# Optimization experiments

Hardware: AMD Instinct MI355X
Metric: run time of the kernel (lower is better)

Reference implementation:

```python
import jax, jax.numpy as jnp
import numpy as np

B, N, F, E, K, R, H = 16, 2048, 2048, 128, 10, 2, 2


def setup_inputs() -> dict:
    key = jax.random.key(0)
    ks = jax.random.split(key, 11)
    s = 0.1  # keep embeddings close so the Gaussian kernel does not underflow
    rel = jax.random.normal(ks[0], (B, E), jnp.float32) * s
    arg1 = jax.random.normal(ks[1], (B, E), jnp.float32) * s
    arg2 = jax.random.normal(ks[2], (B, E), jnp.float32) * s
    fact_rel = jax.random.normal(ks[3], (B, F, E), jnp.float32) * s
    fact_arg1 = jax.random.normal(ks[4], (B, F, E), jnp.float32) * s
    fact_arg2 = jax.random.normal(ks[5], (B, F, E), jnp.float32) * s
    entity_embeddings = jax.random.normal(ks[6], (B, N, E), jnp.float32) * s
    hop_W = jax.random.normal(ks[7], (R, H, E, E), jnp.float32) / jnp.sqrt(jnp.float32(E))
    hop_b = jax.random.normal(ks[8], (R, H, E), jnp.float32) * 0.01
    nb_facts = jax.random.randint(ks[9], (B,), F // 2, F + 1, jnp.int32)
    nb_entities = jax.random.randint(ks[10], (B,), N // 2, N + 1, jnp.int32)
    return dict(rel=rel, arg1=arg1, arg2=arg2, fact_rel=fact_rel,
                fact_arg1=fact_arg1, fact_arg2=fact_arg2,
                entity_embeddings=entity_embeddings, hop_W=hop_W, hop_b=hop_b,
                nb_facts=nb_facts, nb_entities=nb_entities)


def reference(rel, arg1, arg2, fact_rel, fact_arg1, fact_arg2,
              entity_embeddings, hop_W, hop_b, nb_facts, nb_entities):
    # Gaussian kernel k(x,y) = exp(-||x-y||^2 / 2), batched: x [B,T,E], y [B,F,E] -> [B,T,F]
    def kern(x, y):
        d2 = (jnp.sum(x * x, -1)[:, :, None] + jnp.sum(y * y, -1)[:, None, :]
              - 2.0 * jnp.einsum('bte,bfe->btf', x, y))
        return jnp.exp(-0.5 * d2)

    fact_mask = (jnp.arange(F) < nb_facts[:, None])[:, None, :]            # [B,1,F]
    ent_mask = (jnp.arange(N) < nb_entities[:, None]).astype(rel.dtype)    # [B,N]

    # BatchNeuralKB.score: max over (valid) facts of product of kernels. [B,T,E]x3 -> [B,T]
    def model_score(r, a1, a2):
        s = kern(r, fact_rel) * kern(a1, fact_arg1) * kern(a2, fact_arg2)  # [B,T,F]
        return jnp.max(jnp.where(fact_mask, s, 0.0), axis=-1)

    # BatchNeuralKB.forward, (s,p,?) -> score per candidate object entity. [B,1,E] -> [B,N]
    def forward_sp(r, a1):
        kr = jnp.where(fact_mask, kern(r, fact_rel) * kern(a1, fact_arg1), 0.0)  # [B,1,F]
        kE = kern(entity_embeddings, fact_arg2)                                  # [B,N,F]
        return jnp.max(kr * kE, axis=-1) * ent_mask                              # [B,N]

    # (?,p,o) -> score per candidate subject entity
    def forward_po(r, a2):
        kr = jnp.where(fact_mask, kern(r, fact_rel) * kern(a2, fact_arg2), 0.0)
        kE = kern(entity_embeddings, fact_arg1)
        return jnp.max(kr * kE, axis=-1) * ent_mask

    # r_score(depth=1) = max(depth_r_score(0), depth_r_score(1))
    # depth_r_score(0) == model.score
    scores_0 = model_score(rel[:, None], arg1[:, None], arg2[:, None])[:, 0]  # [B]

    global_res = None
    for r_idx in range(R):
        is_rev = (r_idx % 2 == 1)
        # LinearReformulator: hop relations from rel
        h1 = rel @ hop_W[r_idx, 0] + hop_b[r_idx, 0]  # [B,E]
        h2 = rel @ hop_W[r_idx, 1] + hop_b[r_idx, 1]
        # hop 1: r_hop -> scores over all entities, then top-k beam
        if is_rev:
            sp = forward_po(h1[:, None], arg1[:, None])  # [B,N]
        else:
            sp = forward_sp(h1[:, None], arg1[:, None])
        z_scores, z_idx = jax.lax.top_k(sp, K)                                  # [B,K]
        z_emb = jnp.take_along_axis(entity_embeddings, z_idx[:, :, None], axis=1)  # [B,K,E]
        # final hop: r_score(depth=0) == model.score with branched args
        h2k = jnp.broadcast_to(h2[:, None, :], (B, K, E))
        a2k = jnp.broadcast_to(arg2[:, None, :], (B, K, E))
        if is_rev:
            s2 = model_score(h2k, a2k, z_emb)  # [B,K]
        else:
            s2 = model_score(h2k, z_emb, a2k)
        rule_scores = jnp.minimum(s2, z_scores)   # tnorm = 'min'
        rule_res = jnp.max(rule_scores, axis=1)   # max over branches [B]
        global_res = rule_res if global_res is None else jnp.maximum(global_res, rule_res)

    return jnp.maximum(scores_0, global_res)
```

## Files before the change

kernel.cpp:

```cpp
#include <hip/hip_runtime.h>
#include <math.h>

#define Bb 16
#define Nn 2048
#define Ff 2048
#define Ee 128
#define Kk 10
#define S2FC 8
#define S2F (Ff / S2FC)

typedef __attribute__((ext_vector_type(8))) short short8;
typedef __attribute__((ext_vector_type(4))) float f32x4;
typedef unsigned int u32;

__device__ inline float wave_sum(float x) {
    for (int o = 32; o; o >>= 1) x += __shfl_down(x, o);
    return x;
}

__device__ inline void bsplit(float x, unsigned short& h, unsigned short& l) {
    unsigned int u = __float_as_uint(x);
    h = (unsigned short)(u >> 16);
    float hf = __uint_as_float(u & 0xFFFF0000u);
    l = (unsigned short)(__float_as_uint(x - hf) >> 16);
}

__device__ inline void atomic_fmax_pos(float* addr, float v) {
    atomicMax((unsigned int*)addr, __float_as_uint(v));
}

__device__ inline void gload_lds16(const void* g, void* l) {
    __builtin_amdgcn_global_load_lds(
        (const __attribute__((address_space(1))) u32*)g,
        (__attribute__((address_space(3))) u32*)l, 16, 0, 0);
}


__global__ __launch_bounds__(256) void k_pfe(
    const float* __restrict__ rel, const float* __restrict__ arg1,
    const float* __restrict__ arg2, const float* __restrict__ frel,
    const float* __restrict__ fa1, const float* __restrict__ fa2,
    const float* __restrict__ ent, const float* __restrict__ hop_W,
    const float* __restrict__ hop_b, const int* __restrict__ nb_facts,
    unsigned short* __restrict__ B0, unsigned short* __restrict__ B1,
    float* __restrict__ ent_norm, float* __restrict__ c0, float* __restrict__ c1,
    float* __restrict__ s2b0, float* __restrict__ s2b1,
    float* __restrict__ sp0, float* __restrict__ sp1, float* __restrict__ out) {
    int bx = blockIdx.x;
    int tid = threadIdx.x;
    if (bx < 128) {
        int fcb = bx & 7, b = bx >> 3;
        int nbf = nb_facts[b];
        if (fcb * 256 >= nbf) {
            int f = fcb * 256 + tid;
            size_t o = (size_t)b * Ff + f;
            const float NI = -INFINITY;
            c0[o] = NI; c1[o] = NI; s2b0[o] = NI; s2b1[o] = NI;
            return;
        }
        __shared__ float q[7][Ee];
        __shared__ float bred[4];
        if (tid < 128) {
            q[0][tid] = rel[b * Ee + tid];
            q[1][tid] = arg1[b * Ee + tid];
            q[2][tid] = arg2[b * Ee + tid];
        }
        __syncthreads();
        {
            int e = tid & 127, hf = tid >> 7;
            const float* W0 = hop_W + (size_t)(hf * 2) * Ee * Ee;
            const float* W1 = W0 + (size_t)Ee * Ee;
            float a0 = hop_b[(hf * 2) * Ee + e];
            float a1 = hop_b[(hf * 2 + 1) * Ee + e];
            for (int qq = 0; qq < Ee; ++qq) {
                float rq = q[0][qq];
                a0 += rq * W0[qq * Ee + e];
                a1 += rq * W1[qq * Ee + e];
            }
            q[3 + hf][e] = a0;
            q[5 + hf][e] = a1;
        }
        __syncthreads();

        int f = fcb * 256 + tid;
        const float* pr = frel + ((size_t)b * Ff + f) * Ee;
        const float* p1 = fa1 + ((size_t)b * Ff + f) * Ee;
        const float* p2 = fa2 + ((size_t)b * Ff + f) * Ee;
        float d_rr = 0, d_a11 = 0, d_a22 = 0, d_h10 = 0, d_h11 = 0, d_h20 = 0, d_h21 = 0;
        float d_a12 = 0, d_a21 = 0, n1 = 0, n2 = 0;
#pragma unroll 8
        for (int e0 = 0; e0 < Ee; e0 += 4) {
            float4 vr4 = *(const float4*)(pr + e0);
            float4 v14 = *(const float4*)(p1 + e0);
            float4 v24 = *(const float4*)(p2 + e0);
            const float* vrp = (const float*)&vr4;
            const float* v1p = (const float*)&v14;
            const float* v2p = (const float*)&v24;
#pragma unroll
            for (int j = 0; j < 4; ++j) {
                int e = e0 + j;
                float fr = vrp[j], f1 = v1p[j], f2 = v2p[j];
                float t;
                t = q[0][e] - fr; d_rr  += t * t;
                t = q[1][e] - f1; d_a11 += t * t;
                t = q[2][e] - f2; d_a22 += t * t;
                t = q[3][e] - fr; d_h10 += t * t;
                t = q[4][e] - fr; d_h11 += t * t;
                t = q[5][e] - fr; d_h20 += t * t;
                t = q[6][e] - fr; d_h21 += t * t;
                t = q[1][e] - f2; d_a12 += t * t;
                t = q[2][e] - f1; d_a21 += t * t;
                n1 += f1 * f1; n2 += f2 * f2;
            }
        }
        bool valid = f < nbf;
        const float NI = -INFINITY;
        size_t o = (size_t)b * Ff + f;
        c0[o]   = valid ? (-0.5f * (d_h10 + d_a11 + n2)) : NI;
        c1[o]   = valid ? (-0.5f * (d_h11 + d_a12 + n1)) : NI;
        s2b0[o] = valid ? (-0.5f * (d_h20 + d_a22)) : NI;
        s2b1[o] = valid ? (-0.5f * (d_h21 + d_a21)) : NI;
        float lsc = valid ? (-0.5f * (d_rr + d_a11 + d_a22)) : NI;
        for (int m = 32; m; m >>= 1) lsc = fmaxf(lsc, __shfl_down(lsc, m));
        if ((tid & 63) == 0) bred[tid >> 6] = lsc;
        __syncthreads();
        if (tid == 0) {
            float m = fmaxf(fmaxf(bred[0], bred[1]), fmaxf(bred[2], bred[3]));
            atomic_fmax_pos(out + b, expf(m));
        }
    } else if (bx < 128 + 4096) {
        __shared__ uint4 tlds[16 * 33];
        int bxx = bx - 128;
        int y = bxx >> 11, bxi = bxx & 2047;
        int oct = tid & 15, fl = tid >> 4;
        int b = bxi >> 7, fbase = (bxi & 127) * 16;
        const float* src = (y == 0) ? fa2 : fa1;
        const float* s = src + ((size_t)b * Ff + fbase + fl) * Ee + oct * 8;
        float4 v0 = *(const float4*)s;
        float4 v1 = *(const float4*)(s + 4);
        float xs[8] = {v0.x, v0.y, v0.z, v0.w, v1.x, v1.y, v1.z, v1.w};
        unsigned short hi[8], lo[8];
#pragma unroll
        for (int j = 0; j < 8; ++j) bsplit(xs[j], hi[j], lo[j]);
        uint4 ph, pl;
        ph.x = (unsigned)hi[0] | ((unsigned)hi[1] << 16);
        ph.y = (unsigned)hi[2] | ((unsigned)hi[3] << 16);
        ph.z = (unsigned)hi[4] | ((unsigned)hi[5] << 16);
        ph.w = (unsigned)hi[6] | ((unsigned)hi[7] << 16);
        pl.x = (unsigned)lo[0] | ((unsigned)lo[1] << 16);
        pl.y = (unsigned)lo[2] | ((unsigned)lo[3] << 16);
        pl.z = (unsigned)lo[4] | ((unsigned)lo[5] << 16);
        pl.w = (unsigned)lo[6] | ((unsigned)lo[7] << 16);
        tlds[fl * 33 + oct * 2]     = ph;
        tlds[fl * 33 + oct * 2 + 1] = pl;
        __syncthreads();
        int F4 = (fbase >> 4) & 1, F5 = (fbase >> 5) & 1;
        unsigned char* ob = (unsigned char*)((y == 0) ? B0 : B1) +
                            (((size_t)b << 20) + (size_t)(fbase >> 6) * 32768 +
                             F5 * 1024 + F4 * 512);
#pragma unroll
        for (int uu = 0; uu < 2; ++uu) {
            int u = tid + uu * 256;
            int o = u >> 5, sS = u & 31;
            int s0 = sS & 1, s1 = (sS >> 1) & 1, s2 = (sS >> 2) & 1;
            int s3 = (sS >> 3) & 1, s4 = (sS >> 4) & 1;
            int part = s0 ^ s3;
            int fll = (s1 ^ s4) | ((s2 ^ F4) << 1) | (s3 << 2) | (s4 << 3);
            *(uint4*)(ob + o * 2048 + sS * 16) = tlds[fll * 33 + o * 2 + part];
        }
    } else {
        int row  = (bx - (128 + 4096)) * 4 + (tid >> 6);
        int lane = tid & 63;
        const float* p = ent + (size_t)row * Ee;
        float a = p[lane], c = p[lane + 64];
        float s = wave_sum(a * a + c * c);
        if (lane == 0) {
            ent_norm[row] = s;
            sp0[row] = 0.0f;
            sp1[row] = 0.0f;
        }
    }
}

#define BMs 256

__global__ __launch_bounds__(512, 2) void k_spmax_mfma(
    const float* __restrict__ ent, const unsigned short* __restrict__ B0,
    const unsigned short* __restrict__ B1, const float* __restrict__ c0,
    const float* __restrict__ c1, const float* __restrict__ ent_norm,
    const int* __restrict__ nb_facts, const int* __restrict__ nb_entities,
    float* __restrict__ sp0, float* __restrict__ sp1) {
    int bid = blockIdx.x;
    int br = bid & 31, nblk = bid >> 5;
    int b = br >> 1, r = br & 1;
    const unsigned short* Bt = (r == 0) ? B0 : B1;
    const float* cb = ((r == 0) ? c0 : c1) + (size_t)b * Ff;
    float* sp = ((r == 0) ? sp0 : sp1) + (size_t)b * Nn;

    int tid = threadIdx.x;
    int ne = nb_entities[b];
    if (nblk * BMs >= ne) return;
    int nch = (nb_facts[b] + 63) >> 6;

    __shared__ uint4 ldsB4[2 * 2048];

    int wave = tid >> 6, lane = tid & 63;
    int wm = wave >> 1, wn = wave & 1;
    int lane15 = lane & 15, quad = lane >> 4;

    short8 ah[4][4], al[4][4];
    {
        const float* abase = ent + ((size_t)b * Nn + (size_t)nblk * BMs + wm * 64) * Ee;
#pragma unroll
        for (int i = 0; i < 4; ++i)
#pragma unroll
            for (int ks = 0; ks < 4; ++ks) {
                const float* p = abase + (size_t)(i * 16 + lane15) * Ee + ks * 32 + quad * 8;
                float4 v0 = *(const float4*)p;
                float4 v1 = *(const float4*)(p + 4);
                float xs[8] = {v0.x, v0.y, v0.z, v0.w, v1.x, v1.y, v1.z, v1.w};
                short8 hi8, lo8;
#pragma unroll
                for (int j = 0; j < 8; ++j) {
                    unsigned short hh, ll;
                    bsplit(xs[j], hh, ll);
                    hi8[j] = (short)hh;
                    lo8[j] = (short)ll;
                }
                ah[i][ks] = hi8;
                al[i][ks] = lo8;
            }
    }

    int offA = (wn * 32 + lane15) * 32;
    int physA0 = offA ^ (((offA >> 7) & 7) << 4);
    int offB = offA + 512;
    int physB0 = offB ^ (((offB >> 7) & 7) << 4);
    int qoff = quad * 2048;

    unsigned char* ldsB = (unsigned char*)ldsB4;
    const unsigned char* gB = (const unsigned char*)Bt + ((size_t)b << 20);

#pragma unroll
    for (int t = 0; t < 4; ++t) {
        int seg = t * 8 + wave;
        gload_lds16(gB + seg * 1024 + lane * 16, ldsB + seg * 1024);
    }
    __syncthreads();

    float mmax[4][4];
#pragma unroll
    for (int i = 0; i < 4; ++i)
#pragma unroll
        for (int rr = 0; rr < 4; ++rr) mmax[i][rr] = -INFINITY;

    int cur = 0;
    for (int c = 0; c < nch; ++c) {
        if (c + 1 < nch) {
            const unsigned char* gc = gB + (size_t)(c + 1) * 32768;
            unsigned char* lb = ldsB + (cur ^ 1) * 32768;
#pragma unroll
            for (int t = 0; t < 4; ++t) {
                int seg = t * 8 + wave;
                gload_lds16(gc + seg * 1024 + lane * 16, lb + seg * 1024);
            }
        }
        float cj0 = cb[c * 64 + wn * 32 + lane15];
        float cj1 = cb[c * 64 + wn * 32 + 16 + lane15];
        f32x4 acc[4][2];
#pragma unroll
        for (int i = 0; i < 4; ++i) {
            acc[i][0] = (f32x4){cj0, cj0, cj0, cj0};
            acc[i][1] = (f32x4){cj1, cj1, cj1, cj1};
        }
        const unsigned char* bb = ldsB + cur * 32768;
#pragma unroll
        for (int ks = 0; ks < 4; ++ks) {
            const unsigned char* bk = bb + ks * 8192 + qoff;
            short8 bh0 = *(const short8*)(bk + physA0);
            short8 bl0 = *(const short8*)(bk + (physA0 ^ 16));
            short8 bh1 = *(const short8*)(bk + physB0);
            short8 bl1 = *(const short8*)(bk + (physB0 ^ 16));
#pragma unroll
            for (int i = 0; i < 4; ++i) {
                acc[i][0] = __builtin_amdgcn_mfma_f32_16x16x32_bf16(ah[i][ks], bh0, acc[i][0], 0, 0, 0);
                acc[i][0] = __builtin_amdgcn_mfma_f32_16x16x32_bf16(al[i][ks], bh0, acc[i][0], 0, 0, 0);
                acc[i][0] = __builtin_amdgcn_mfma_f32_16x16x32_bf16(ah[i][ks], bl0, acc[i][0], 0, 0, 0);
                acc[i][1] = __builtin_amdgcn_mfma_f32_16x16x32_bf16(ah[i][ks], bh1, acc[i][1], 0, 0, 0);
                acc[i][1] = __builtin_amdgcn_mfma_f32_16x16x32_bf16(al[i][ks], bh1, acc[i][1], 0, 0, 0);
                acc[i][1] = __builtin_amdgcn_mfma_f32_16x16x32_bf16(ah[i][ks], bl1, acc[i][1], 0, 0, 0);
            }
        }

#pragma unroll
        for (int j = 0; j < 2; ++j)
#pragma unroll
            for (int i = 0; i < 4; ++i)
#pragma unroll
                for (int rr = 0; rr < 4; ++rr)
                    mmax[i][rr] = fmaxf(mmax[i][rr], acc[i][j][rr]);

        __syncthreads();
        cur ^= 1;
    }

    float* red = (float*)ldsB;
#pragma unroll
    for (int i = 0; i < 4; ++i)
#pragma unroll
        for (int rr = 0; rr < 4; ++rr) {
            float v = mmax[i][rr];
#pragma unroll
            for (int m = 1; m < 16; m <<= 1) v = fmaxf(v, __shfl_xor(v, m));
            if (lane15 == 0) red[(wm * 64 + i * 16 + quad * 4 + rr) * 2 + wn] = v;
        }
    __syncthreads();
    if (tid < BMs) {
        float m = fmaxf(red[tid * 2], red[tid * 2 + 1]);
        int n = nblk * BMs + tid;
        if (n < ne)
            sp[n] = expf(m - 0.5f * ent_norm[(size_t)b * Nn + n]);
    }
}

__global__ __launch_bounds__(256) void k_s2t(
    const float* __restrict__ ent, const float* __restrict__ fa1,
    const float* __restrict__ fa2, const float* __restrict__ s2b0,
    const float* __restrict__ s2b1, const float* __restrict__ sp0,
    const float* __restrict__ sp1, const int* __restrict__ nb_facts,
    float* __restrict__ out) {
    int fc = blockIdx.x, b = blockIdx.y, r = blockIdx.z;
    if (fc * S2F >= nb_facts[b]) return;
    const float* factX = (r == 0) ? fa1 : fa2;
    const float* s2b   = ((r == 0) ? s2b0 : s2b1) + (size_t)b * Ff;
    const float* sp    = ((r == 0) ? sp0 : sp1) + (size_t)b * Nn;

    __shared__ float zsc[Kk];
    __shared__ int   zidx[Kk];
    __shared__ float zsh[Kk][Ee];
    __shared__ float znorm[Kk];
    __shared__ float red[4][Kk];
    __shared__ float rules[Kk];

    int tid = threadIdx.x;
    int wv = tid >> 6, lane = tid & 63;

    if (wv == 0) {
        float v[Nn / 64];
#pragma unroll
        for (int i = 0; i < Nn / 64; ++i) v[i] = sp[i * 64 + lane];
        for (int k = 0; k < Kk; ++k) {
            float best = -INFINITY; int bidx = 0;
#pragma unroll
            for (int i = 0; i < Nn / 64; ++i)
                if (v[i] > best) { best = v[i]; bidx = i * 64 + lane; }
#pragma unroll
            for (int m = 1; m < 64; m <<= 1) {
                float ov = __shfl_xor(best, m);
                int oi = __shfl_xor(bidx, m);
                if (ov > best || (ov == best && oi < bidx)) { best = ov; bidx = oi; }
            }
            if (lane == 0) { zsc[k] = best; zidx[k] = bidx; }
            if ((bidx & 63) == lane) {
                int slot = bidx >> 6;
#pragma unroll
                for (int i = 0; i < Nn / 64; ++i)
                    if (i == slot) v[i] = -INFINITY;
            }
        }
    }
    __syncthreads();
    for (int idx = tid; idx < Kk * Ee; idx += 256) {
        int k = idx >> 7, e = idx & 127;
        zsh[k][e] = ent[((size_t)b * Nn + zidx[k]) * Ee + e];
    }
    __syncthreads();
    if (tid < Kk) {
        float s = 0.f;
        for (int e = 0; e < Ee; ++e) { float v = zsh[tid][e]; s += v * v; }
        znorm[tid] = s;
    }
    __syncthreads();

    int f = fc * S2F + tid;
    const float* fp = factX + ((size_t)b * Ff + f) * Ee;
    float acc[Kk];
#pragma unroll
    for (int k = 0; k < Kk; ++k) acc[k] = 0.f;
    float nf = 0.f;
#pragma unroll 4
    for (int e0 = 0; e0 < Ee; e0 += 4) {
        float4 v = *(const float4*)(fp + e0);
        nf += v.x * v.x + v.y * v.y + v.z * v.z + v.w * v.w;
#pragma unroll
        for (int k = 0; k < Kk; ++k) {
            float4 z = *(const float4*)&zsh[k][e0];
            acc[k] += z.x * v.x + z.y * v.y + z.z * v.z + z.w * v.w;
        }
    }
    float base = s2b[f] - 0.5f * nf;
    float sc[Kk];
#pragma unroll
    for (int k = 0; k < Kk; ++k) sc[k] = base + acc[k] - 0.5f * znorm[k];
    for (int o = 32; o; o >>= 1)
#pragma unroll
        for (int k = 0; k < Kk; ++k) sc[k] = fmaxf(sc[k], __shfl_down(sc[k], o));
    if ((tid & 63) == 0)
#pragma unroll
        for (int k = 0; k < Kk; ++k) red[wv][k] = sc[k];
    __syncthreads();
    if (tid < Kk) {
        float m = fmaxf(fmaxf(red[0][tid], red[1][tid]), fmaxf(red[2][tid], red[3][tid]));
        rules[tid] = fminf(expf(m), zsc[tid]);
    }
    __syncthreads();
    if (tid == 0) {
        float g = rules[0];
#pragma unroll
        for (int k = 1; k < Kk; ++k) g = fmaxf(g, rules[k]);
        atomic_fmax_pos(out + b, g);
    }
}

extern "C" void kernel_launch(void* const* d_in, const int* in_sizes, int n_in,
                              void* d_out, int out_size, void* d_ws, size_t ws_size,
                              hipStream_t stream) {
    const float* rel  = (const float*)d_in[0];
    const float* arg1 = (const float*)d_in[1];
    const float* arg2 = (const float*)d_in[2];
    const float* frel = (const float*)d_in[3];
    const float* fa1  = (const float*)d_in[4];
    const float* fa2  = (const float*)d_in[5];
    const float* ent  = (const float*)d_in[6];
    const float* hopW = (const float*)d_in[7];
    const float* hopb = (const float*)d_in[8];
    const int* nb_facts    = (const int*)d_in[9];
    const int* nb_entities = (const int*)d_in[10];
    float* out = (float*)d_out;

    float* ws = (float*)d_ws;
    size_t off = 0;
    float* c0       = ws + off; off += (size_t)Bb * Ff;
    float* c1       = ws + off; off += (size_t)Bb * Ff;
    float* s2b0     = ws + off; off += (size_t)Bb * Ff;
    float* s2b1     = ws + off; off += (size_t)Bb * Ff;
    float* sp0      = ws + off; off += (size_t)Bb * Nn;
    float* sp1      = ws + off; off += (size_t)Bb * Nn;
    float* ent_norm = ws + off; off += (size_t)Bb * Nn;
    off = (off + 7) & ~(size_t)7;
    unsigned short* B0 = (unsigned short*)(ws + off); off += (size_t)Bb * 16 * Ff * 8;
    unsigned short* B1 = (unsigned short*)(ws + off); off += (size_t)Bb * 16 * Ff * 8;

    hipMemsetAsync(d_out, 0, (size_t)out_size * sizeof(float), stream);
    k_pfe<<<dim3(128 + 4096 + Bb * Nn / 4), 256, 0, stream>>>(
        rel, arg1, arg2, frel, fa1, fa2, ent, hopW, hopb, nb_facts,
        B0, B1, ent_norm, c0, c1, s2b0, s2b1, sp0, sp1, out);
    k_spmax_mfma<<<dim3(32 * 8), 512, 0, stream>>>(ent, B0, B1, c0, c1, ent_norm,
                                                   nb_facts, nb_entities, sp0, sp1);
    k_s2t<<<dim3(S2FC, Bb, 2), 256, 0, stream>>>(ent, fa1, fa2, s2b0, s2b1,
                                                 sp0, sp1, nb_facts, out);
}
```

Before: 225.5 us.

## Deepen B-operand pipeline to four LDS buffers with explicit vmcnt waits

The MFMA spmax kernel now stages fact chunks two ahead into a four-slot LDS ring, waiting on explicit vmcnt counts with one barrier per chunk instead of double buffering. The packed B layout written by the prep kernel is reordered so each lane reads contiguous 16-byte fragments at fixed offsets, which removes the XOR swizzle address math. The per-fact constants are preloaded into LDS once per block. LDS use grows to about 136 KB per block, which risks occupancy with two 512-thread blocks per CU. The unswizzled layout may also cause bank conflicts.

```diff
diff --git a/kernel.cpp b/kernel.cpp
--- a/kernel.cpp
+++ b/kernel.cpp
@@ -157,16 +157,13 @@
         int F4 = (fbase >> 4) & 1, F5 = (fbase >> 5) & 1;
         unsigned char* ob = (unsigned char*)((y == 0) ? B0 : B1) +
                             (((size_t)b << 20) + (size_t)(fbase >> 6) * 32768 +
-                             F5 * 1024 + F4 * 512);
+                             F5 * 4096 + F4 * 2048);
 #pragma unroll
         for (int uu = 0; uu < 2; ++uu) {
             int u = tid + uu * 256;
-            int o = u >> 5, sS = u & 31;
-            int s0 = sS & 1, s1 = (sS >> 1) & 1, s2 = (sS >> 2) & 1;
-            int s3 = (sS >> 3) & 1, s4 = (sS >> 4) & 1;
-            int part = s0 ^ s3;
-            int fll = (s1 ^ s4) | ((s2 ^ F4) << 1) | (s3 << 2) | (s4 << 3);
-            *(uint4*)(ob + o * 2048 + sS * 16) = tlds[fll * 33 + o * 2 + part];
+            int fl2 = u & 15, qd = (u >> 4) & 3, p = (u >> 6) & 1, ks = u >> 7;
+            *(uint4*)(ob + ks * 8192 + p * 1024 + qd * 256 + fl2 * 16) =
+                tlds[fl2 * 33 + (ks * 4 + qd) * 2 + p];
         }
     } else {
         int row  = (bx - (128 + 4096)) * 4 + (tid >> 6);
@@ -202,7 +199,8 @@
     if (nblk * BMs >= ne) return;
     int nch = (nb_facts[b] + 63) >> 6;
 
-    __shared__ uint4 ldsB4[2 * 2048];
+    __shared__ uint4 ldsB4[4 * 2048];
+    __shared__ float ldsC[Ff];
 
     int wave = tid >> 6, lane = tid & 63;
     int wm = wave >> 1, wn = wave & 1;
@@ -232,20 +230,23 @@
             }
     }
 
-    int offA = (wn * 32 + lane15) * 32;
-    int physA0 = offA ^ (((offA >> 7) & 7) << 4);
-    int offB = offA + 512;
-    int physB0 = offB ^ (((offB >> 7) & 7) << 4);
-    int qoff = quad * 2048;
-
     unsigned char* ldsB = (unsigned char*)ldsB4;
     const unsigned char* gB = (const unsigned char*)Bt + ((size_t)b << 20);
 
-#pragma unroll
-    for (int t = 0; t < 4; ++t) {
-        int seg = t * 8 + wave;
-        gload_lds16(gB + seg * 1024 + lane * 16, ldsB + seg * 1024);
-    }
+#define STAGE(cc)                                                              \
+    {                                                                          \
+        const unsigned char* gc_ = gB + (size_t)(cc) * 32768;                  \
+        unsigned char* lb_ = ldsB + ((cc) & 3) * 32768;                        \
+        _Pragma("unroll")                                                      \
+        for (int t_ = 0; t_ < 4; ++t_) {                                       \
+            int seg_ = t_ * 8 + wave;                                          \
+            gload_lds16(gc_ + seg_ * 1024 + (lane << 4), lb_ + seg_ * 1024);   \
+        }                                                                      \
+    }
+
+    ((float4*)ldsC)[tid] = ((const float4*)cb)[tid];
+    STAGE(0);
+    STAGE(1);
     __syncthreads();
 
     float mmax[4][4];
@@ -254,33 +255,32 @@
 #pragma unroll
         for (int rr = 0; rr < 4; ++rr) mmax[i][rr] = -INFINITY;
 
-    int cur = 0;
     for (int c = 0; c < nch; ++c) {
-        if (c + 1 < nch) {
-            const unsigned char* gc = gB + (size_t)(c + 1) * 32768;
-            unsigned char* lb = ldsB + (cur ^ 1) * 32768;
-#pragma unroll
-            for (int t = 0; t < 4; ++t) {
-                int seg = t * 8 + wave;
-                gload_lds16(gc + seg * 1024 + lane * 16, lb + seg * 1024);
-            }
-        }
-        float cj0 = cb[c * 64 + wn * 32 + lane15];
-        float cj1 = cb[c * 64 + wn * 32 + 16 + lane15];
+        if (c + 2 < nch) STAGE(c + 2);
+        __builtin_amdgcn_sched_barrier(0);
+        if (c + 2 < nch)      asm volatile("s_waitcnt vmcnt(8)" ::: "memory");
+        else if (c + 1 < nch) asm volatile("s_waitcnt vmcnt(4)" ::: "memory");
+        else                  asm volatile("s_waitcnt vmcnt(0)" ::: "memory");
+        __builtin_amdgcn_sched_barrier(0);
+        __builtin_amdgcn_s_barrier();
+        __builtin_amdgcn_sched_barrier(0);
+
+        float cj0 = ldsC[c * 64 + wn * 32 + lane15];
+        float cj1 = ldsC[c * 64 + wn * 32 + 16 + lane15];
         f32x4 acc[4][2];
 #pragma unroll
         for (int i = 0; i < 4; ++i) {
             acc[i][0] = (f32x4){cj0, cj0, cj0, cj0};
             acc[i][1] = (f32x4){cj1, cj1, cj1, cj1};
         }
-        const unsigned char* bb = ldsB + cur * 32768;
+        const unsigned char* bb = ldsB + (c & 3) * 32768 + wn * 4096 + (lane << 4);
 #pragma unroll
         for (int ks = 0; ks < 4; ++ks) {
-            const unsigned char* bk = bb + ks * 8192 + qoff;
-            short8 bh0 = *(const short8*)(bk + physA0);
-            short8 bl0 = *(const short8*)(bk + (physA0 ^ 16));
-            short8 bh1 = *(const short8*)(bk + physB0);
-            short8 bl1 = *(const short8*)(bk + (physB0 ^ 16));
+            const unsigned char* bk = bb + ks * 8192;
+            short8 bh0 = *(const short8*)(bk);
+            short8 bl0 = *(const short8*)(bk + 1024);
+            short8 bh1 = *(const short8*)(bk + 2048);
+            short8 bl1 = *(const short8*)(bk + 3072);
 #pragma unroll
             for (int i = 0; i < 4; ++i) {
                 acc[i][0] = __builtin_amdgcn_mfma_f32_16x16x32_bf16(ah[i][ks], bh0, acc[i][0], 0, 0, 0);
@@ -299,11 +299,10 @@
 #pragma unroll
                 for (int rr = 0; rr < 4; ++rr)
                     mmax[i][rr] = fmaxf(mmax[i][rr], acc[i][j][rr]);
-
-        __syncthreads();
-        cur ^= 1;
-    }
-
+    }
+#undef STAGE
+
+    __syncthreads();
     float* red = (float*)ldsB;
 #pragma unroll
     for (int i = 0; i < 4; ++i)
```

After: 226.4 us. Within noise of the previous version (+0.4%).

## Stage fact rows through padded LDS with coalesced loads in fact-distance blocks

Applied to the files above, without the earlier changes.

The fact-distance branch of k_pfe now handles 128 facts per block instead of 256, doubling the block count. Each of the three fact arrays is loaded cooperatively with coalesced float4 reads into a padded 128x129 LDS tile. Each thread then reads its own row from LDS, replacing per-thread strided global reads of whole 512-byte rows. The cost is about 66 KB of shared memory per block, which limits occupancy, extra barriers, and only half the threads doing the compute phase.

```diff
diff --git a/kernel.cpp b/kernel.cpp
--- a/kernel.cpp
+++ b/kernel.cpp
@@ -48,17 +48,20 @@
     float* __restrict__ sp0, float* __restrict__ sp1, float* __restrict__ out) {
     int bx = blockIdx.x;
     int tid = threadIdx.x;
-    if (bx < 128) {
-        int fcb = bx & 7, b = bx >> 3;
+    if (bx < 256) {
+        int fcb = bx & 15, b = bx >> 4;
         int nbf = nb_facts[b];
-        if (fcb * 256 >= nbf) {
-            int f = fcb * 256 + tid;
-            size_t o = (size_t)b * Ff + f;
-            const float NI = -INFINITY;
-            c0[o] = NI; c1[o] = NI; s2b0[o] = NI; s2b1[o] = NI;
+        const float NI = -INFINITY;
+        int fbase = fcb * 128;
+        if (fbase >= nbf) {
+            if (tid < 128) {
+                size_t o = (size_t)b * Ff + fbase + tid;
+                c0[o] = NI; c1[o] = NI; s2b0[o] = NI; s2b1[o] = NI;
+            }
             return;
         }
         __shared__ float q[7][Ee];
+        __shared__ float rows[128][129];
         __shared__ float bred[4];
         if (tid < 128) {
             q[0][tid] = rel[b * Ee + tid];
@@ -72,6 +75,7 @@
             const float* W1 = W0 + (size_t)Ee * Ee;
             float a0 = hop_b[(hf * 2) * Ee + e];
             float a1 = hop_b[(hf * 2 + 1) * Ee + e];
+#pragma unroll 8
             for (int qq = 0; qq < Ee; ++qq) {
                 float rq = q[0][qq];
                 a0 += rq * W0[qq * Ee + e];
@@ -80,46 +84,72 @@
             q[3 + hf][e] = a0;
             q[5 + hf][e] = a1;
         }
-        __syncthreads();
-
-        int f = fcb * 256 + tid;
-        const float* pr = frel + ((size_t)b * Ff + f) * Ee;
-        const float* p1 = fa1 + ((size_t)b * Ff + f) * Ee;
-        const float* p2 = fa2 + ((size_t)b * Ff + f) * Ee;
-        float d_rr = 0, d_a11 = 0, d_a22 = 0, d_h10 = 0, d_h11 = 0, d_h20 = 0, d_h21 = 0;
-        float d_a12 = 0, d_a21 = 0, n1 = 0, n2 = 0;
+
+        __syncthreads();
+        for (int idx = tid; idx < 128 * 32; idx += 256) {
+            int row = idx >> 5, c4 = (idx & 31) * 4;
+            float4 v = *(const float4*)(frel + ((size_t)b * Ff + fbase + row) * Ee + c4);
+            rows[row][c4] = v.x; rows[row][c4 + 1] = v.y;
+            rows[row][c4 + 2] = v.z; rows[row][c4 + 3] = v.w;
+        }
+        __syncthreads();
+        float d_rr = 0, d_h10 = 0, d_h11 = 0, d_h20 = 0, d_h21 = 0;
+        if (tid < 128) {
 #pragma unroll 8
-        for (int e0 = 0; e0 < Ee; e0 += 4) {
-            float4 vr4 = *(const float4*)(pr + e0);
-            float4 v14 = *(const float4*)(p1 + e0);
-            float4 v24 = *(const float4*)(p2 + e0);
-            const float* vrp = (const float*)&vr4;
-            const float* v1p = (const float*)&v14;
-            const float* v2p = (const float*)&v24;
-#pragma unroll
-            for (int j = 0; j < 4; ++j) {
-                int e = e0 + j;
-                float fr = vrp[j], f1 = v1p[j], f2 = v2p[j];
-                float t;
+            for (int e = 0; e < Ee; ++e) {
+                float fr = rows[tid][e], t;
                 t = q[0][e] - fr; d_rr  += t * t;
-                t = q[1][e] - f1; d_a11 += t * t;
-                t = q[2][e] - f2; d_a22 += t * t;
                 t = q[3][e] - fr; d_h10 += t * t;
                 t = q[4][e] - fr; d_h11 += t * t;
                 t = q[5][e] - fr; d_h20 += t * t;
                 t = q[6][e] - fr; d_h21 += t * t;
+            }
+        }
+        __syncthreads();
+        for (int idx = tid; idx < 128 * 32; idx += 256) {
+            int row = idx >> 5, c4 = (idx & 31) * 4;
+            float4 v = *(const float4*)(fa1 + ((size_t)b * Ff + fbase + row) * Ee + c4);
+            rows[row][c4] = v.x; rows[row][c4 + 1] = v.y;
+            rows[row][c4 + 2] = v.z; rows[row][c4 + 3] = v.w;
+        }
+        __syncthreads();
+        float d_a11 = 0, d_a21 = 0, n1 = 0;
+        if (tid < 128) {
+#pragma unroll 8
+            for (int e = 0; e < Ee; ++e) {
+                float f1 = rows[tid][e], t;
+                t = q[1][e] - f1; d_a11 += t * t;
+                t = q[2][e] - f1; d_a21 += t * t;
+                n1 += f1 * f1;
+            }
+        }
+        __syncthreads();
+        for (int idx = tid; idx < 128 * 32; idx += 256) {
+            int row = idx >> 5, c4 = (idx & 31) * 4;
+            float4 v = *(const float4*)(fa2 + ((size_t)b * Ff + fbase + row) * Ee + c4);
+            rows[row][c4] = v.x; rows[row][c4 + 1] = v.y;
+            rows[row][c4 + 2] = v.z; rows[row][c4 + 3] = v.w;
+        }
+        __syncthreads();
+        float d_a22 = 0, d_a12 = 0, n2 = 0;
+        if (tid < 128) {
+#pragma unroll 8
+            for (int e = 0; e < Ee; ++e) {
+                float f2 = rows[tid][e], t;
+                t = q[2][e] - f2; d_a22 += t * t;
                 t = q[1][e] - f2; d_a12 += t * t;
-                t = q[2][e] - f1; d_a21 += t * t;
-                n1 += f1 * f1; n2 += f2 * f2;
-            }
-        }
-        bool valid = f < nbf;
-        const float NI = -INFINITY;
-        size_t o = (size_t)b * Ff + f;
-        c0[o]   = valid ? (-0.5f * (d_h10 + d_a11 + n2)) : NI;
-        c1[o]   = valid ? (-0.5f * (d_h11 + d_a12 + n1)) : NI;
-        s2b0[o] = valid ? (-0.5f * (d_h20 + d_a22)) : NI;
-        s2b1[o] = valid ? (-0.5f * (d_h21 + d_a21)) : NI;
+                n2 += f2 * f2;
+            }
+        }
+
+        bool valid = (tid < 128) && (fbase + tid < nbf);
+        if (tid < 128) {
+            size_t o = (size_t)b * Ff + fbase + tid;
+            c0[o]   = valid ? (-0.5f * (d_h10 + d_a11 + n2)) : NI;
+            c1[o]   = valid ? (-0.5f * (d_h11 + d_a12 + n1)) : NI;
+            s2b0[o] = valid ? (-0.5f * (d_h20 + d_a22)) : NI;
+            s2b1[o] = valid ? (-0.5f * (d_h21 + d_a21)) : NI;
+        }
         float lsc = valid ? (-0.5f * (d_rr + d_a11 + d_a22)) : NI;
         for (int m = 32; m; m >>= 1) lsc = fmaxf(lsc, __shfl_down(lsc, m));
         if ((tid & 63) == 0) bred[tid >> 6] = lsc;
@@ -128,9 +158,9 @@
             float m = fmaxf(fmaxf(bred[0], bred[1]), fmaxf(bred[2], bred[3]));
             atomic_fmax_pos(out + b, expf(m));
         }
-    } else if (bx < 128 + 4096) {
+    } else if (bx < 256 + 4096) {
         __shared__ uint4 tlds[16 * 33];
-        int bxx = bx - 128;
+        int bxx = bx - 256;
         int y = bxx >> 11, bxi = bxx & 2047;
         int oct = tid & 15, fl = tid >> 4;
         int b = bxi >> 7, fbase = (bxi & 127) * 16;
@@ -169,7 +199,7 @@
             *(uint4*)(ob + o * 2048 + sS * 16) = tlds[fll * 33 + o * 2 + part];
         }
     } else {
-        int row  = (bx - (128 + 4096)) * 4 + (tid >> 6);
+        int row  = (bx - (256 + 4096)) * 4 + (tid >> 6);
         int lane = tid & 63;
         const float* p = ent + (size_t)row * Ee;
         float a = p[lane], c = p[lane + 64];
@@ -452,7 +482,7 @@
     unsigned short* B1 = (unsigned short*)(ws + off); off += (size_t)Bb * 16 * Ff * 8;
 
     hipMemsetAsync(d_out, 0, (size_t)out_size * sizeof(float), stream);
-    k_pfe<<<dim3(128 + 4096 + Bb * Nn / 4), 256, 0, stream>>>(
+    k_pfe<<<dim3(256 + 4096 + Bb * Nn / 4), 256, 0, stream>>>(
         rel, arg1, arg2, frel, fa1, fa2, ent, hopW, hopb, nb_facts,
         B0, B1, ent_norm, c0, c1, s2b0, s2b1, sp0, sp1, out);
     k_spmax_mfma<<<dim3(32 * 8), 512, 0, stream>>>(ent, B0, B1, c0, c1, ent_norm,
```

Measured after the change: 226.5 us, median of 2. Within noise of the previous version (+0.5%).
